# Kernel optimization log

Hardware: AMD Instinct MI355X
Metric: run time of the kernel (lower is better)

The kernel has to match this reference:

```python
import jax, jax.numpy as jnp
import numpy as np

N_NODES = 50000


def gcn_conv(x, edge_index, W, b, n_nodes):
    """PyG GCNConv: add self-loops, symmetric deg normalization, gather-scatter."""
    src, dst = edge_index[0], edge_index[1]
    loop = jnp.arange(n_nodes, dtype=src.dtype)
    src = jnp.concatenate([src, loop])
    dst = jnp.concatenate([dst, loop])
    # transform first (in -> hidden), then propagate
    h = x @ W  # [N, H]
    ones = jnp.ones_like(dst, dtype=h.dtype)
    deg = jax.ops.segment_sum(ones, dst, num_segments=n_nodes)  # [N]
    dinv = jnp.where(deg > 0, jax.lax.rsqrt(deg), 0.0)
    norm = dinv[src] * dinv[dst]  # [E+N]
    msg = h[src] * norm[:, None]  # [E+N, H] gather + scale
    out = jax.ops.segment_sum(msg, dst, num_segments=n_nodes)  # scatter-add
    return out + b


def setup_inputs() -> dict:
    key = jax.random.key(0)
    ks = jax.random.split(key, 5)
    N, E, C_in, H, C_out = N_NODES, 800000, 128, 128, 1
    x = jax.random.normal(ks[0], (N, C_in), dtype=jnp.float32)
    edge_index = jax.random.randint(ks[1], (2, E), 0, N, dtype=jnp.int32)
    sc_in = 1.0 / np.sqrt(C_in)
    sc_h = 1.0 / np.sqrt(H)
    W_gcn = jax.random.normal(ks[2], (C_in, H), dtype=jnp.float32) * sc_in
    b_gcn = jnp.zeros((H,), dtype=jnp.float32)
    W1 = jax.random.normal(ks[3], (H, H), dtype=jnp.float32) * sc_h
    b1 = jnp.zeros((H,), dtype=jnp.float32)
    W2 = jax.random.normal(ks[4], (H, C_out), dtype=jnp.float32) * sc_h
    b2 = jnp.zeros((C_out,), dtype=jnp.float32)
    return {"x": x, "edge_index": edge_index, "W_gcn": W_gcn, "b_gcn": b_gcn,
            "W1": W1, "b1": b1, "W2": W2, "b2": b2}


def reference(x, edge_index, W_gcn, b_gcn, W1, b1, W2, b2):
    n_nodes = x.shape[0]
    h = jax.nn.relu(gcn_conv(x, edge_index, W_gcn, b_gcn, n_nodes))
    h = jax.nn.relu(h @ W1 + b1)
    return h @ W2 + b2
```

## Files before the change

kernel.cpp:

```cpp
#include <hip/hip_runtime.h>
#include <hip/hip_bf16.h>

#define HID 128
#define EPB 2048
#define BSH 6
#define CAP 1280
#define NBMAX 800
#define SROW 136

typedef __attribute__((ext_vector_type(8))) short bf16x8;
typedef __attribute__((ext_vector_type(4))) float f32x4;

static inline size_t align256(size_t x) { return (x + 255) & ~(size_t)255; }

__device__ __forceinline__ unsigned short f2bf(float f) {
    unsigned int u = __float_as_uint(f);
    unsigned int r = (u + 0x7fffu + ((u >> 16) & 1u)) >> 16;
    return (unsigned short)r;
}
__device__ __forceinline__ float bf2f(unsigned short h) {
    return __uint_as_float(((unsigned int)h) << 16);
}
__device__ __forceinline__ float2 bf2x2(unsigned int u) {
    return make_float2(__uint_as_float(u << 16), __uint_as_float(u & 0xffff0000u));
}

__global__ void k_prep(const float* __restrict__ W, const float* __restrict__ W1,
                       unsigned short* __restrict__ WT, unsigned short* __restrict__ W1T,
                       int* __restrict__ deg, int* __restrict__ gbase, int N, int nbuck) {
    int idx = blockIdx.x * 256 + threadIdx.x;
    if (idx < HID * HID) {
        int k = idx >> 7, n = idx & 127;
        WT[n * HID + k]  = f2bf(W[idx]);
        W1T[n * HID + k] = f2bf(W1[idx]);
    }
    if (idx < N) deg[idx] = 0;
    if (idx < nbuck) gbase[idx] = idx * CAP;
}

__global__ __launch_bounds__(256) void k_gemm_bin(
        const float* __restrict__ x, const unsigned short* __restrict__ WT,
        unsigned short* __restrict__ hs, int N,
        const int* __restrict__ src, const int* __restrict__ dst, int E,
        int* __restrict__ gbase, unsigned int* __restrict__ ebuf,
        int* __restrict__ deg, int nbuck, int gemm_blocks) {
    __shared__ int sh_h[NBMAX], sh_cur[NBMAX];
    int bid = blockIdx.x;
    if (bid < gemm_blocks) {
        int tid = threadIdx.x;
        int wid = tid >> 6, lane = tid & 63;
        int m = lane & 15, q = lane >> 4;
        int row0 = bid * 64 + wid * 16;
        int arow_i = row0 + m;
        bool rvalid = arow_i < N;
        const float* arow = x + (size_t)arow_i * HID;
        f32x4 acc[8];
#pragma unroll
        for (int t = 0; t < 8; t++) acc[t] = (f32x4){0.f, 0.f, 0.f, 0.f};
#pragma unroll
        for (int c = 0; c < 4; c++) {
            bf16x8 a;
            if (rvalid) {
                float4 f0 = *(const float4*)(arow + c * 32 + q * 8);
                float4 f1 = *(const float4*)(arow + c * 32 + q * 8 + 4);
                a = (bf16x8){(short)f2bf(f0.x), (short)f2bf(f0.y), (short)f2bf(f0.z), (short)f2bf(f0.w),
                             (short)f2bf(f1.x), (short)f2bf(f1.y), (short)f2bf(f1.z), (short)f2bf(f1.w)};
            } else {
                a = (bf16x8){0, 0, 0, 0, 0, 0, 0, 0};
            }
#pragma unroll
            for (int t = 0; t < 8; t++) {
                bf16x8 b = *(const bf16x8*)(WT + (size_t)(t * 16 + m) * HID + c * 32 + q * 8);
                acc[t] = __builtin_amdgcn_mfma_f32_16x16x32_bf16(a, b, acc[t], 0, 0, 0);
            }
        }
#pragma unroll
        for (int t = 0; t < 8; t++) {
#pragma unroll
            for (int r = 0; r < 4; r++) {
                int rr = row0 + q * 4 + r;
                if (rr < N) hs[(size_t)rr * HID + t * 16 + m] = f2bf(acc[t][r]);
            }
        }
        return;
    }
    int blk = bid - gemm_blocks;
    int t = threadIdx.x;
    for (int i = t; i < nbuck; i += 256) sh_h[i] = 0;
    __syncthreads();
    int e0 = blk * EPB;
    bool full = (e0 + EPB <= E);
    int s[8], d[8];
    if (full) {
        int4 sa = ((const int4*)(src + e0))[t * 2];
        int4 sb = ((const int4*)(src + e0))[t * 2 + 1];
        int4 da = ((const int4*)(dst + e0))[t * 2];
        int4 db = ((const int4*)(dst + e0))[t * 2 + 1];
        s[0] = sa.x; s[1] = sa.y; s[2] = sa.z; s[3] = sa.w;
        s[4] = sb.x; s[5] = sb.y; s[6] = sb.z; s[7] = sb.w;
        d[0] = da.x; d[1] = da.y; d[2] = da.z; d[3] = da.w;
        d[4] = db.x; d[5] = db.y; d[6] = db.z; d[7] = db.w;
    } else {
#pragma unroll
        for (int i = 0; i < 8; i++) {
            int e = e0 + t * 8 + i;
            s[i] = (e < E) ? src[e] : 0;
            d[i] = (e < E) ? dst[e] : 0;
        }
    }
#pragma unroll
    for (int i = 0; i < 8; i++) {
        int e = e0 + t * 8 + i;
        if (e < E) {
            atomicAdd(&sh_h[d[i] >> BSH], 1);
            atomicAdd(&deg[d[i]], 1);
        }
    }
    __syncthreads();
    for (int i = t; i < nbuck; i += 256) {
        int v = sh_h[i];
        if (v) sh_cur[i] = atomicAdd(&gbase[i], v);
    }
    __syncthreads();
#pragma unroll
    for (int i = 0; i < 8; i++) {
        int e = e0 + t * 8 + i;
        if (e < E) {
            int b = d[i] >> BSH;
            int p = atomicAdd(&sh_cur[b], 1);
            ebuf[p] = (unsigned int)s[i] | ((unsigned int)d[i] << 16);
        }
    }
}

__global__ __launch_bounds__(256) void k_prop_mlp(
        const unsigned short* __restrict__ hs,
        const unsigned int* __restrict__ ebuf, const int* __restrict__ gbase,
        const int* __restrict__ deg,
        const float* __restrict__ b_gcn,
        const unsigned short* __restrict__ W1T,
        const float* __restrict__ b1, const float* __restrict__ W2,
        const float* __restrict__ b2,
        float* __restrict__ out, int N) {
    __shared__ int sE[CAP];
    __shared__ int scnt[64], scur[64], srow0[64];
    __shared__ __align__(16) unsigned short stage[64 * SROW];
    __shared__ float sb1[128], sW2[128];
    int k = blockIdx.x, tid = threadIdx.x;
    int node0 = k << BSH;
    int wid = tid >> 6, lane = tid & 63;
    int g = lane >> 4;
    int fl = lane & 15;

    if (tid < 64) scnt[tid] = 0;
    if (tid < 128) { sb1[tid] = b1[tid]; sW2[tid] = W2[tid]; }
    __syncthreads();

    int e0 = k * CAP, e1 = gbase[k];
    unsigned int ue[5];
#pragma unroll
    for (int i = 0; i < 5; i++) {
        int e = e0 + tid + i * 256;
        ue[i] = (e < e1) ? ebuf[e] : 0xffffffffu;
    }
#pragma unroll
    for (int i = 0; i < 5; i++)
        if (ue[i] != 0xffffffffu) atomicAdd(&scnt[(ue[i] >> 16) & 63u], 1);
    __syncthreads();
    if (tid < 64) {
        int v = scnt[tid];
        int sc = v;
#pragma unroll
        for (int off = 1; off < 64; off <<= 1) {
            int u = __shfl_up(sc, off);
            if (tid >= off) sc += u;
        }
        int excl = sc - v;
        scur[tid] = excl;
        srow0[tid] = excl;
    }
    __syncthreads();
#pragma unroll
    for (int i = 0; i < 5; i++) {
        if (ue[i] != 0xffffffffu) {
            int r = (int)((ue[i] >> 16) & 63u);
            int pos = atomicAdd(&scur[r], 1);
            sE[pos] = (int)(ue[i] & 0xffffu);
        }
    }
    __syncthreads();

    const uint4* hsv = (const uint4*)hs;
    float4 b0 = *(const float4*)(b_gcn + fl * 8);
    float4 b1v = *(const float4*)(b_gcn + fl * 8 + 4);
    for (int r = wid * 16; r < wid * 16 + 16; r++) {
        int s0 = srow0[r], s1 = scur[r];
        int node = node0 + r;
        bool rv = node < N;
        float di = rv ? rsqrtf((float)deg[node] + 1.0f) : 0.f;
        float a0 = 0.f, a1 = 0.f, a2 = 0.f, a3 = 0.f, a4 = 0.f, a5 = 0.f, a6 = 0.f, a7 = 0.f;
        int j = s0;
        for (; j + 16 <= s1; j += 16) {
            int eA = sE[j + g], eB = sE[j + 4 + g];
            int eC = sE[j + 8 + g], eD = sE[j + 12 + g];
            float dA = rsqrtf((float)deg[eA] + 1.f);
            float dB = rsqrtf((float)deg[eB] + 1.f);
            float dC = rsqrtf((float)deg[eC] + 1.f);
            float dD = rsqrtf((float)deg[eD] + 1.f);
            uint4 uA = hsv[(size_t)eA * 16 + fl];
            uint4 uB = hsv[(size_t)eB * 16 + fl];
            uint4 uC = hsv[(size_t)eC * 16 + fl];
            uint4 uD = hsv[(size_t)eD * 16 + fl];
            float2 f;
            f = bf2x2(uA.x); a0 += dA * f.x; a1 += dA * f.y;
            f = bf2x2(uA.y); a2 += dA * f.x; a3 += dA * f.y;
            f = bf2x2(uA.z); a4 += dA * f.x; a5 += dA * f.y;
            f = bf2x2(uA.w); a6 += dA * f.x; a7 += dA * f.y;
            f = bf2x2(uB.x); a0 += dB * f.x; a1 += dB * f.y;
            f = bf2x2(uB.y); a2 += dB * f.x; a3 += dB * f.y;
            f = bf2x2(uB.z); a4 += dB * f.x; a5 += dB * f.y;
            f = bf2x2(uB.w); a6 += dB * f.x; a7 += dB * f.y;
            f = bf2x2(uC.x); a0 += dC * f.x; a1 += dC * f.y;
            f = bf2x2(uC.y); a2 += dC * f.x; a3 += dC * f.y;
            f = bf2x2(uC.z); a4 += dC * f.x; a5 += dC * f.y;
            f = bf2x2(uC.w); a6 += dC * f.x; a7 += dC * f.y;
            f = bf2x2(uD.x); a0 += dD * f.x; a1 += dD * f.y;
            f = bf2x2(uD.y); a2 += dD * f.x; a3 += dD * f.y;
            f = bf2x2(uD.z); a4 += dD * f.x; a5 += dD * f.y;
            f = bf2x2(uD.w); a6 += dD * f.x; a7 += dD * f.y;
        }
        for (; j + 8 <= s1; j += 8) {
            int eA = sE[j + g], eB = sE[j + 4 + g];
            float dA = rsqrtf((float)deg[eA] + 1.f);
            float dB = rsqrtf((float)deg[eB] + 1.f);
            uint4 uA = hsv[(size_t)eA * 16 + fl];
            uint4 uB = hsv[(size_t)eB * 16 + fl];
            float2 f;
            f = bf2x2(uA.x); a0 += dA * f.x; a1 += dA * f.y;
            f = bf2x2(uA.y); a2 += dA * f.x; a3 += dA * f.y;
            f = bf2x2(uA.z); a4 += dA * f.x; a5 += dA * f.y;
            f = bf2x2(uA.w); a6 += dA * f.x; a7 += dA * f.y;
            f = bf2x2(uB.x); a0 += dB * f.x; a1 += dB * f.y;
            f = bf2x2(uB.y); a2 += dB * f.x; a3 += dB * f.y;
            f = bf2x2(uB.z); a4 += dB * f.x; a5 += dB * f.y;
            f = bf2x2(uB.w); a6 += dB * f.x; a7 += dB * f.y;
        }
        for (; j + g < s1; j += 4) {
            int ei = sE[j + g];
            float dA = rsqrtf((float)deg[ei] + 1.f);
            uint4 u = hsv[(size_t)ei * 16 + fl];
            float2 f;
            f = bf2x2(u.x); a0 += dA * f.x; a1 += dA * f.y;
            f = bf2x2(u.y); a2 += dA * f.x; a3 += dA * f.y;
            f = bf2x2(u.z); a4 += dA * f.x; a5 += dA * f.y;
            f = bf2x2(u.w); a6 += dA * f.x; a7 += dA * f.y;
        }
        if (g == 0 && rv) {
            uint4 u = hsv[(size_t)node * 16 + fl];
            float2 f;
            f = bf2x2(u.x); a0 += di * f.x; a1 += di * f.y;
            f = bf2x2(u.y); a2 += di * f.x; a3 += di * f.y;
            f = bf2x2(u.z); a4 += di * f.x; a5 += di * f.y;
            f = bf2x2(u.w); a6 += di * f.x; a7 += di * f.y;
        }
#pragma unroll
        for (int off = 16; off <= 32; off <<= 1) {
            a0 += __shfl_xor(a0, off); a1 += __shfl_xor(a1, off);
            a2 += __shfl_xor(a2, off); a3 += __shfl_xor(a3, off);
            a4 += __shfl_xor(a4, off); a5 += __shfl_xor(a5, off);
            a6 += __shfl_xor(a6, off); a7 += __shfl_xor(a7, off);
        }
        if (g == 0) {
            uint4 o;
            o.x = (unsigned int)f2bf(fmaxf(di * a0 + b0.x, 0.f)) | ((unsigned int)f2bf(fmaxf(di * a1 + b0.y, 0.f)) << 16);
            o.y = (unsigned int)f2bf(fmaxf(di * a2 + b0.z, 0.f)) | ((unsigned int)f2bf(fmaxf(di * a3 + b0.w, 0.f)) << 16);
            o.z = (unsigned int)f2bf(fmaxf(di * a4 + b1v.x, 0.f)) | ((unsigned int)f2bf(fmaxf(di * a5 + b1v.y, 0.f)) << 16);
            o.w = (unsigned int)f2bf(fmaxf(di * a6 + b1v.z, 0.f)) | ((unsigned int)f2bf(fmaxf(di * a7 + b1v.w, 0.f)) << 16);
            *(uint4*)(stage + r * SROW + fl * 8) = o;
        }
    }

    int m = lane & 15, q = lane >> 4;
    int row = wid * 16 + m;
    f32x4 acc[8];
#pragma unroll
    for (int t = 0; t < 8; t++) acc[t] = (f32x4){0.f, 0.f, 0.f, 0.f};
#pragma unroll
    for (int c = 0; c < 4; c++) {
        bf16x8 a = *(const bf16x8*)(stage + row * SROW + c * 32 + q * 8);
#pragma unroll
        for (int t = 0; t < 8; t++) {
            bf16x8 b = *(const bf16x8*)(W1T + (size_t)(t * 16 + m) * HID + c * 32 + q * 8);
            acc[t] = __builtin_amdgcn_mfma_f32_16x16x32_bf16(a, b, acc[t], 0, 0, 0);
        }
    }
    float part[4] = {0.f, 0.f, 0.f, 0.f};
#pragma unroll
    for (int t = 0; t < 8; t++) {
        int nc = t * 16 + m;
        float w2 = sW2[nc], bb = sb1[nc];
#pragma unroll
        for (int r2 = 0; r2 < 4; r2++)
            part[r2] += fmaxf(acc[t][r2] + bb, 0.f) * w2;
    }
#pragma unroll
    for (int off = 8; off >= 1; off >>= 1) {
#pragma unroll
        for (int r2 = 0; r2 < 4; r2++) part[r2] += __shfl_xor(part[r2], off);
    }
    if (m == 0) {
        float bb = b2[0];
#pragma unroll
        for (int r2 = 0; r2 < 4; r2++) {
            int rr = node0 + wid * 16 + q * 4 + r2;
            if (rr < N) out[rr] = part[r2] + bb;
        }
    }
}

extern "C" void kernel_launch(void* const* d_in, const int* in_sizes, int n_in,
                              void* d_out, int out_size, void* d_ws, size_t ws_size,
                              hipStream_t stream) {
    const float* x     = (const float*)d_in[0];
    const int*   ei    = (const int*)d_in[1];
    const float* W_gcn = (const float*)d_in[2];
    const float* b_gcn = (const float*)d_in[3];
    const float* W1    = (const float*)d_in[4];
    const float* b1    = (const float*)d_in[5];
    const float* W2    = (const float*)d_in[6];
    const float* b2    = (const float*)d_in[7];
    float* out = (float*)d_out;

    int N = in_sizes[0] / HID;
    int E = in_sizes[1] / 2;
    const int* e_src = ei;
    const int* e_dst = ei + E;
    int NBUCK = (N + 63) >> BSH;
    int NBLK = (E + EPB - 1) / EPB;

    char* ws = (char*)d_ws;
    size_t off = 0;
    unsigned short* hs = (unsigned short*)(ws + off);      off = align256(off + (size_t)N * HID * 2);
    int* deg = (int*)(ws + off);                           off = align256(off + (size_t)N * 4);
    int* gbase = (int*)(ws + off);                         off = align256(off + (size_t)NBUCK * 4);
    unsigned int* ebuf = (unsigned int*)(ws + off);        off = align256(off + (size_t)NBUCK * CAP * 4);
    unsigned short* WT = (unsigned short*)(ws + off);      off = align256(off + (size_t)HID * HID * 2);
    unsigned short* W1T = (unsigned short*)(ws + off);     off = align256(off + (size_t)HID * HID * 2);

    int mfma_blocks = (N + 63) / 64;

    k_prep<<<(N + 255) / 256, 256, 0, stream>>>(W_gcn, W1, WT, W1T, deg, gbase, N, NBUCK);

    k_gemm_bin<<<mfma_blocks + NBLK, 256, 0, stream>>>(x, WT, hs, N, e_src, e_dst, E,
                                                       gbase, ebuf, deg, NBUCK, mfma_blocks);

    k_prop_mlp<<<NBUCK, 256, 0, stream>>>(hs, ebuf, gbase, deg, b_gcn, W1T, b1, W2, b2, out, N);
}
```

Before: 188.4 us.

## Compute degree normalization from bucketed edges in separate kernel instead of global atomics

Removes the per-edge global atomicAdd on the degree array during binning. Degrees are now counted per bucket in shared memory by a new kernel that reads the already-bucketed edge buffer, and it stores precomputed rsqrt values. The propagation kernel then loads dinv directly instead of recomputing rsqrt per neighbor. The cost is one extra kernel launch and another pass over the edge buffer. The deg zeroing in the prep kernel goes away, so prep now launches fewer blocks.

```diff
diff --git a/kernel.cpp b/kernel.cpp
--- a/kernel.cpp
+++ b/kernel.cpp
@@ -27,14 +27,13 @@
 
 __global__ void k_prep(const float* __restrict__ W, const float* __restrict__ W1,
                        unsigned short* __restrict__ WT, unsigned short* __restrict__ W1T,
-                       int* __restrict__ deg, int* __restrict__ gbase, int N, int nbuck) {
+                       int* __restrict__ gbase, int nbuck) {
     int idx = blockIdx.x * 256 + threadIdx.x;
     if (idx < HID * HID) {
         int k = idx >> 7, n = idx & 127;
         WT[n * HID + k]  = f2bf(W[idx]);
         W1T[n * HID + k] = f2bf(W1[idx]);
     }
-    if (idx < N) deg[idx] = 0;
     if (idx < nbuck) gbase[idx] = idx * CAP;
 }
 
@@ -43,7 +42,7 @@
         unsigned short* __restrict__ hs, int N,
         const int* __restrict__ src, const int* __restrict__ dst, int E,
         int* __restrict__ gbase, unsigned int* __restrict__ ebuf,
-        int* __restrict__ deg, int nbuck, int gemm_blocks) {
+        int nbuck, int gemm_blocks) {
     __shared__ int sh_h[NBMAX], sh_cur[NBMAX];
     int bid = blockIdx.x;
     if (bid < gemm_blocks) {
@@ -111,10 +110,7 @@
 #pragma unroll
     for (int i = 0; i < 8; i++) {
         int e = e0 + t * 8 + i;
-        if (e < E) {
-            atomicAdd(&sh_h[d[i] >> BSH], 1);
-            atomicAdd(&deg[d[i]], 1);
-        }
+        if (e < E) atomicAdd(&sh_h[d[i] >> BSH], 1);
     }
     __syncthreads();
     for (int i = t; i < nbuck; i += 256) {
@@ -133,10 +129,30 @@
     }
 }
 
+__global__ __launch_bounds__(256) void k_dinv(const unsigned int* __restrict__ ebuf,
+                                              const int* __restrict__ gbase,
+                                              float* __restrict__ dinv, int N) {
+    __shared__ int cnt[64];
+    int k = blockIdx.x, t = threadIdx.x;
+    if (t < 64) cnt[t] = 0;
+    __syncthreads();
+    int e0 = k * CAP, e1 = gbase[k];
+#pragma unroll
+    for (int i = 0; i < 5; i++) {
+        int e = e0 + t + i * 256;
+        if (e < e1) atomicAdd(&cnt[(ebuf[e] >> 16) & 63u], 1);
+    }
+    __syncthreads();
+    if (t < 64) {
+        int node = (k << BSH) + t;
+        if (node < N) dinv[node] = rsqrtf((float)cnt[t] + 1.0f);
+    }
+}
+
 __global__ __launch_bounds__(256) void k_prop_mlp(
         const unsigned short* __restrict__ hs,
         const unsigned int* __restrict__ ebuf, const int* __restrict__ gbase,
-        const int* __restrict__ deg,
+        const float* __restrict__ dinv,
         const float* __restrict__ b_gcn,
         const unsigned short* __restrict__ W1T,
         const float* __restrict__ b1, const float* __restrict__ W2,
@@ -197,16 +213,13 @@
         int s0 = srow0[r], s1 = scur[r];
         int node = node0 + r;
         bool rv = node < N;
-        float di = rv ? rsqrtf((float)deg[node] + 1.0f) : 0.f;
+        float di = rv ? dinv[node] : 0.f;
         float a0 = 0.f, a1 = 0.f, a2 = 0.f, a3 = 0.f, a4 = 0.f, a5 = 0.f, a6 = 0.f, a7 = 0.f;
         int j = s0;
         for (; j + 16 <= s1; j += 16) {
             int eA = sE[j + g], eB = sE[j + 4 + g];
             int eC = sE[j + 8 + g], eD = sE[j + 12 + g];
-            float dA = rsqrtf((float)deg[eA] + 1.f);
-            float dB = rsqrtf((float)deg[eB] + 1.f);
-            float dC = rsqrtf((float)deg[eC] + 1.f);
-            float dD = rsqrtf((float)deg[eD] + 1.f);
+            float dA = dinv[eA], dB = dinv[eB], dC = dinv[eC], dD = dinv[eD];
             uint4 uA = hsv[(size_t)eA * 16 + fl];
             uint4 uB = hsv[(size_t)eB * 16 + fl];
             uint4 uC = hsv[(size_t)eC * 16 + fl];
@@ -231,8 +244,7 @@
         }
         for (; j + 8 <= s1; j += 8) {
             int eA = sE[j + g], eB = sE[j + 4 + g];
-            float dA = rsqrtf((float)deg[eA] + 1.f);
-            float dB = rsqrtf((float)deg[eB] + 1.f);
+            float dA = dinv[eA], dB = dinv[eB];
             uint4 uA = hsv[(size_t)eA * 16 + fl];
             uint4 uB = hsv[(size_t)eB * 16 + fl];
             float2 f;
@@ -247,7 +259,7 @@
         }
         for (; j + g < s1; j += 4) {
             int ei = sE[j + g];
-            float dA = rsqrtf((float)deg[ei] + 1.f);
+            float dA = dinv[ei];
             uint4 u = hsv[(size_t)ei * 16 + fl];
             float2 f;
             f = bf2x2(u.x); a0 += dA * f.x; a1 += dA * f.y;
@@ -341,7 +353,7 @@
     char* ws = (char*)d_ws;
     size_t off = 0;
     unsigned short* hs = (unsigned short*)(ws + off);      off = align256(off + (size_t)N * HID * 2);
-    int* deg = (int*)(ws + off);                           off = align256(off + (size_t)N * 4);
+    float* dinv = (float*)(ws + off);                      off = align256(off + (size_t)N * 4);
     int* gbase = (int*)(ws + off);                         off = align256(off + (size_t)NBUCK * 4);
     unsigned int* ebuf = (unsigned int*)(ws + off);        off = align256(off + (size_t)NBUCK * CAP * 4);
     unsigned short* WT = (unsigned short*)(ws + off);      off = align256(off + (size_t)HID * HID * 2);
@@ -349,10 +361,12 @@
 
     int mfma_blocks = (N + 63) / 64;
 
-    k_prep<<<(N + 255) / 256, 256, 0, stream>>>(W_gcn, W1, WT, W1T, deg, gbase, N, NBUCK);
+    k_prep<<<(HID * HID + 255) / 256, 256, 0, stream>>>(W_gcn, W1, WT, W1T, gbase, NBUCK);
 
     k_gemm_bin<<<mfma_blocks + NBLK, 256, 0, stream>>>(x, WT, hs, N, e_src, e_dst, E,
-                                                       gbase, ebuf, deg, NBUCK, mfma_blocks);
-
-    k_prop_mlp<<<NBUCK, 256, 0, stream>>>(hs, ebuf, gbase, deg, b_gcn, W1T, b1, W2, b2, out, N);
-}
+                                                       gbase, ebuf, NBUCK, mfma_blocks);
+
+    k_dinv<<<NBUCK, 256, 0, stream>>>(ebuf, gbase, dinv, N);
+
+    k_prop_mlp<<<NBUCK, 256, 0, stream>>>(hs, ebuf, gbase, dinv, b_gcn, W1T, b1, W2, b2, out, N);
+}
```

Measured after the change: 163.6 us. 13.2% less time.
